# Kernel optimization log

Hardware: AMD Instinct MI355X
Metric: run time of the kernel (lower is better)

Reference implementation:

```python
import jax, jax.numpy as jnp
import numpy as np

# Problem sizes
N, E, G = 100000, 400000, 2048      # nodes, edges, graphs
NIN, H, NHID, NOUT = 300, 256, 512, 768
NL, T = 3, 16                        # extra atom GAT layers (num_layers=4), pooling timesteps
SLOPE = 0.01                         # leaky_relu negative slope (PyG AttentiveFP uses 0.01)


def setup_inputs() -> dict:
    ks = iter(jax.random.split(jax.random.key(0), 80))
    def rn(shape, s=0.1):
        return jax.random.normal(next(ks), shape, dtype=jnp.float32) * s
    inp = {
        "x": rn((N, NIN), 1.0),
        "edge_attr": rn((E, 1), 1.0),
        # learned parameters (inference mode: dropout disabled)
        "lin1_W": rn((H, NIN)), "lin1_b": rn((H,)),
        # GATEConv
        "g_lin1_W": rn((H, H + 1)), "g_lin2_W": rn((H, H)),
        "g_att_l": rn((H,)), "g_att_r": rn((H,)), "g_bias": rn((H,)),
        "gru0_wih": rn((3 * H, H)), "gru0_whh": rn((3 * H, H)),
        "gru0_bih": rn((3 * H,)), "gru0_bhh": rn((3 * H,)),
        # 3 atom GATConv layers (stacked)
        "atom_W": rn((NL, H, H)), "atom_att_src": rn((NL, H)),
        "atom_att_dst": rn((NL, H)), "atom_bias": rn((NL, H)),
        "agru_wih": rn((NL, 3 * H, H)), "agru_whh": rn((NL, 3 * H, H)),
        "agru_bih": rn((NL, 3 * H)), "agru_bhh": rn((NL, 3 * H)),
        # molecule-level GATConv + GRU (16 timesteps)
        "mol_W": rn((H, H)), "mol_att_src": rn((H,)),
        "mol_att_dst": rn((H,)), "mol_bias": rn((H,)),
        "mgru_wih": rn((3 * H, H)), "mgru_whh": rn((3 * H, H)),
        "mgru_bih": rn((3 * H,)), "mgru_bhh": rn((3 * H,)),
        "lin2_W": rn((NHID, H)), "lin2_b": rn((NHID,)),
        "fc1_W": rn((NOUT, NHID)), "fc1_b": rn((NOUT,)),
        # int inputs
        "edge_index": jax.random.randint(next(ks), (2, E), 0, N),
        "batch": jnp.sort(jax.random.randint(next(ks), (N,), 0, G)),
    }
    return inp


def _lrelu(x):
    return jnp.where(x >= 0, x, SLOPE * x)


def _gru(xin, h, wih, whh, bih, bhh):
    gi = xin @ wih.T + bih
    gh = h @ whh.T + bhh
    ir, iz, inn = jnp.split(gi, 3, axis=-1)
    hr, hz, hn = jnp.split(gh, 3, axis=-1)
    r = jax.nn.sigmoid(ir + hr)
    z = jax.nn.sigmoid(iz + hz)
    n = jnp.tanh(inn + r * hn)
    return (1.0 - z) * n + z * h


def _seg_softmax(a, idx, n):
    m = jax.ops.segment_max(a, idx, num_segments=n)
    e = jnp.exp(a - m[idx])
    s = jax.ops.segment_sum(e, idx, num_segments=n)
    return e / s[idx]


def reference(x, edge_attr, lin1_W, lin1_b, g_lin1_W, g_lin2_W, g_att_l, g_att_r,
              g_bias, gru0_wih, gru0_whh, gru0_bih, gru0_bhh, atom_W, atom_att_src,
              atom_att_dst, atom_bias, agru_wih, agru_whh, agru_bih, agru_bhh,
              mol_W, mol_att_src, mol_att_dst, mol_bias, mgru_wih, mgru_whh,
              mgru_bih, mgru_bhh, lin2_W, lin2_b, fc1_W, fc1_b, edge_index, batch):
    src, dst = edge_index[0], edge_index[1]
    # input projection
    x = _lrelu(x @ lin1_W.T + lin1_b)                                   # [N, H]
    # GATEConv: edge-feature attention
    ge = _lrelu(jnp.concatenate([x[src], edge_attr], axis=-1) @ g_lin1_W.T)  # [E, H]
    a = _lrelu(ge @ g_att_l + (x @ g_att_r)[dst])                       # [E]
    alpha = _seg_softmax(a, dst, N)
    h = jax.ops.segment_sum((x[src] @ g_lin2_W.T) * alpha[:, None], dst,
                            num_segments=N) + g_bias
    x = jax.nn.relu(_gru(jax.nn.elu(h), x, gru0_wih, gru0_whh, gru0_bih, gru0_bhh))
    # remaining atom GATConv + GRU layers
    for l in range(NL):
        xw = x @ atom_W[l].T                                            # [N, H]
        a = _lrelu((xw @ atom_att_src[l])[src] + (xw @ atom_att_dst[l])[dst])
        alpha = _seg_softmax(a, dst, N)
        h = jax.ops.segment_sum(xw[src] * alpha[:, None], dst,
                                num_segments=N) + atom_bias[l]
        x = jax.nn.relu(_gru(jax.nn.elu(h), x, agru_wih[l], agru_whh[l],
                             agru_bih[l], agru_bhh[l]))
    # attentive global pooling (node -> graph bipartite GAT, 16 timesteps)
    out = jax.nn.relu(jax.ops.segment_sum(x, batch, num_segments=G))    # [G, H]
    xw = x @ mol_W.T                                                    # shared lin for src/dst
    a_src = xw @ mol_att_src                                            # [N]
    for _ in range(T):
        a = _lrelu(a_src + ((out @ mol_W.T) @ mol_att_dst)[batch])      # [N]
        alpha = _seg_softmax(a, batch, G)
        h = jax.ops.segment_sum(xw * alpha[:, None], batch,
                                num_segments=G) + mol_bias
        out = jax.nn.relu(_gru(jax.nn.elu(h), out, mgru_wih, mgru_whh,
                               mgru_bih, mgru_bhh))
    out = out @ lin2_W.T + lin2_b                                       # [G, NHID]
    # encoder head: relu -> (global_mean_pool is identity on graph-level emb) -> fc1
    return jax.nn.relu(out) @ fc1_W.T + fc1_b                           # [G, NOUT]
```

## Files before the change

kernel.cpp:

```cpp
#include <hip/hip_runtime.h>
#include <hip/hip_bf16.h>
#include <math.h>

typedef __attribute__((ext_vector_type(8))) short           short8;
typedef __attribute__((ext_vector_type(8))) unsigned short  ushort8;
typedef __attribute__((ext_vector_type(4))) unsigned short  us4;
typedef __attribute__((ext_vector_type(4))) float           f32x4;

__device__ __forceinline__ float lreluf(float v){ return v >= 0.f ? v : 0.01f*v; }
__device__ __forceinline__ float sigf(float v){ return 1.f/(1.f + expf(-v)); }

#define OP_NONE  0
#define OP_LRELU 1
#define OP_RELU  2

__device__ __forceinline__ float applyOp(float v, int op){
  if (op == OP_LRELU) return v >= 0.f ? v : 0.01f*v;
  if (op == OP_RELU)  return v > 0.f ? v : 0.f;
  return v;
}

__device__ __forceinline__ unsigned short f2b(float f){
  unsigned x = __float_as_uint(f);
  unsigned lsb = (x >> 16) & 1u;
  return (unsigned short)((x + 0x7fffu + lsb) >> 16);
}
__device__ __forceinline__ float b2f(unsigned short h){
  return __uint_as_float((unsigned)h << 16);
}
__device__ __forceinline__ void split2(float v, unsigned short& h, unsigned short& l){
  h = f2b(v);
  l = f2b(v - b2f(h));
}
__device__ __forceinline__ float rec2(unsigned short h, unsigned short l){
  return b2f(h) + b2f(l);
}

__device__ __forceinline__ int ldsOff(int row, int chunk){
  return row*32 + ((chunk ^ ((row >> 1) & 3)) << 3);
}

__device__ __forceinline__ float blkSum(float v, float* red){
  int t = threadIdx.x;
  red[t] = v; __syncthreads();
  for (int s = 128; s > 0; s >>= 1){ if (t < s) red[t] += red[t+s]; __syncthreads(); }
  float r = red[0]; __syncthreads();
  return r;
}
__device__ __forceinline__ float blkMax(float v, float* red){
  int t = threadIdx.x;
  red[t] = v; __syncthreads();
  for (int s = 128; s > 0; s >>= 1){ if (t < s) red[t] = fmaxf(red[t], red[t+s]); __syncthreads(); }
  float r = red[0]; __syncthreads();
  return r;
}

__device__ __forceinline__ f32x4 mfma3(short8 aH, short8 aL, short8 bH, short8 bL, f32x4 acc){
  acc = __builtin_amdgcn_mfma_f32_16x16x32_bf16(aL, bH, acc, 0, 0, 0);
  acc = __builtin_amdgcn_mfma_f32_16x16x32_bf16(aH, bL, acc, 0, 0, 0);
  acc = __builtin_amdgcn_mfma_f32_16x16x32_bf16(aH, bH, acc, 0, 0, 0);
  return acc;
}

__global__ void wsplit_k(const float* __restrict__ src, unsigned short* __restrict__ Hd,
                         unsigned short* __restrict__ Ld, int lda, int K, long long tot)
{
  long long i = (long long)blockIdx.x*256 + threadIdx.x;
  if (i >= tot) return;
  long long r = i / K; int c = (int)(i % K);
  float v = src[r*lda + c];
  unsigned short h = f2b(v);
  Hd[r*(long long)K + c] = h;
  Ld[r*(long long)K + c] = f2b(v - b2f(h));
}

__device__ __forceinline__ void stagePS(const unsigned short* __restrict__ GH,
    const unsigned short* __restrict__ GL, int ldk, int row0, int k0,
    unsigned short* __restrict__ ldsH, unsigned short* __restrict__ ldsL, int tid)
{
  int r = tid >> 2, c = tid & 3;
  size_t go = (size_t)(row0 + r)*ldk + k0 + c*8;
  ushort8 vh = *(const ushort8*)&GH[go];
  ushort8 vl = *(const ushort8*)&GL[go];
  int off = ldsOff(r, c);
  *(ushort8*)&ldsH[off] = vh;
  *(ushort8*)&ldsL[off] = vl;
}

__device__ __forceinline__ void stage2(const float* __restrict__ src, int lda,
    int row0, int rowmax, int k0, int K,
    unsigned short* __restrict__ ldsH, unsigned short* __restrict__ ldsL, int tid)
{
  int r = tid >> 2, c = tid & 3;
  int gr = row0 + r, gk = k0 + c*8;
  const float* p = src + (size_t)gr*lda + gk;
  float f[8];
  if (gr < rowmax && gk + 8 <= K && ((lda & 3) == 0)){
    float4 f0 = *(const float4*)p;
    float4 f1 = *(const float4*)(p+4);
    f[0]=f0.x; f[1]=f0.y; f[2]=f0.z; f[3]=f0.w;
    f[4]=f1.x; f[5]=f1.y; f[6]=f1.z; f[7]=f1.w;
  } else {
    #pragma unroll
    for (int j = 0; j < 8; ++j) f[j] = (gr < rowmax && gk + j < K) ? p[j] : 0.f;
  }
  ushort8 vh, vl;
  #pragma unroll
  for (int j = 0; j < 8; ++j){
    unsigned short h, l; split2(f[j], h, l);
    vh[j] = h; vl[j] = l;
  }
  int off = ldsOff(r, c);
  *(ushort8*)&ldsH[off] = vh;
  *(ushort8*)&ldsL[off] = vl;
}

__global__ __launch_bounds__(256) void gemm_mfma_k(
    const float* __restrict__ A, int lda,
    const float* __restrict__ W, int ldw,
    const float* __restrict__ bias,
    unsigned short* __restrict__ CH, unsigned short* __restrict__ CL,
    int M, int N, int K, int op)
{
  __shared__ unsigned short AsH[64*32], AsL[64*32];
  __shared__ unsigned short WsH[64*32], WsL[64*32];
  const int tid = threadIdx.x;
  const int bm = blockIdx.y * 64, bn = blockIdx.x * 64;
  const int wave = tid >> 6, lane = tid & 63;
  const int wr = wave >> 1, wc = wave & 1;
  const int quad = lane >> 4, id = lane & 15;

  f32x4 acc[2][2] = {};
  const int iters = (K + 31) / 32;
  for (int kt = 0; kt < iters; ++kt){
    int k0 = kt * 32;
    stage2(A, lda, bm, M, k0, K, AsH, AsL, tid);
    stage2(W, ldw, bn, N, k0, K, WsH, WsL, tid);
    __syncthreads();
    short8 aH[2], aL[2], bH[2], bL[2];
    #pragma unroll
    for (int i = 0; i < 2; ++i){
      int off = ldsOff(wr*32 + i*16 + id, quad);
      aH[i] = *(const short8*)&AsH[off];
      aL[i] = *(const short8*)&AsL[off];
    }
    #pragma unroll
    for (int j = 0; j < 2; ++j){
      int off = ldsOff(wc*32 + j*16 + id, quad);
      bH[j] = *(const short8*)&WsH[off];
      bL[j] = *(const short8*)&WsL[off];
    }
    #pragma unroll
    for (int i = 0; i < 2; ++i)
      #pragma unroll
      for (int j = 0; j < 2; ++j)
        acc[i][j] = mfma3(aH[i], aL[i], bH[j], bL[j], acc[i][j]);
    __syncthreads();
  }
  #pragma unroll
  for (int i = 0; i < 2; ++i){
    int gr0 = bm + wr*32 + i*16 + quad*4;
    #pragma unroll
    for (int j = 0; j < 2; ++j){
      int gc = bn + wc*32 + j*16 + id;
      if (gc >= N) continue;
      float bv = bias ? bias[gc] : 0.f;
      #pragma unroll
      for (int r = 0; r < 4; ++r){
        int row = gr0 + r;
        if (row >= M) continue;
        float v = applyOp(acc[i][j][r] + bv, op);
        unsigned short h, l; split2(v, h, l);
        CH[(size_t)row*N + gc] = h;
        CL[(size_t)row*N + gc] = l;
      }
    }
  }
}

__global__ __launch_bounds__(256) void gemm_ps_k(
    const unsigned short* __restrict__ AH, const unsigned short* __restrict__ AL,
    const unsigned short* __restrict__ WH_, const unsigned short* __restrict__ WL_,
    const float* __restrict__ bias, float* __restrict__ C,
    unsigned short* __restrict__ CH, unsigned short* __restrict__ CL,
    int M, int N, int K, int op, int ncb)
{
  __shared__ unsigned short AsH[64*32], AsL[64*32];
  __shared__ unsigned short WsH[64*32], WsL[64*32];
  int nwg = gridDim.x, bid = blockIdx.x;
  int q = nwg >> 3, r = nwg & 7;
  int xcd = bid & 7, jj = bid >> 3;
  int idx = (xcd < r ? xcd*(q+1) : r*(q+1) + (xcd - r)*q) + jj;
  const int bm = (idx / ncb)*64, bn = (idx % ncb)*64;
  const int tid = threadIdx.x;
  const int wave = tid >> 6, lane = tid & 63;
  const int wr = wave >> 1, wc = wave & 1;
  const int quad = lane >> 4, id = lane & 15;

  f32x4 acc[2][2] = {};
  const int iters = K >> 5;
  for (int kt = 0; kt < iters; ++kt){
    int k0 = kt * 32;
    stagePS(AH, AL, K, bm, k0, AsH, AsL, tid);
    stagePS(WH_, WL_, K, bn, k0, WsH, WsL, tid);
    __syncthreads();
    short8 aH[2], aL[2], bH[2], bL[2];
    #pragma unroll
    for (int i = 0; i < 2; ++i){
      int off = ldsOff(wr*32 + i*16 + id, quad);
      aH[i] = *(const short8*)&AsH[off];
      aL[i] = *(const short8*)&AsL[off];
    }
    #pragma unroll
    for (int j = 0; j < 2; ++j){
      int off = ldsOff(wc*32 + j*16 + id, quad);
      bH[j] = *(const short8*)&WsH[off];
      bL[j] = *(const short8*)&WsL[off];
    }
    #pragma unroll
    for (int i = 0; i < 2; ++i)
      #pragma unroll
      for (int j = 0; j < 2; ++j)
        acc[i][j] = mfma3(aH[i], aL[i], bH[j], bL[j], acc[i][j]);
    __syncthreads();
  }
  #pragma unroll
  for (int i = 0; i < 2; ++i){
    int gr0 = bm + wr*32 + i*16 + quad*4;
    #pragma unroll
    for (int j = 0; j < 2; ++j){
      int gc = bn + wc*32 + j*16 + id;
      float bv = bias ? bias[gc] : 0.f;
      #pragma unroll
      for (int rr = 0; rr < 4; ++rr){
        int row = gr0 + rr;
        if (row >= M) continue;
        float v = applyOp(acc[i][j][rr] + bv, op);
        if (C)  C[(size_t)row*N + gc] = v;
        if (CH){
          unsigned short h, l; split2(v, h, l);
          CH[(size_t)row*N + gc] = h;
          CL[(size_t)row*N + gc] = l;
        }
      }
    }
  }
}

__global__ __launch_bounds__(256) void gemm2_ps_k(
    const unsigned short* __restrict__ AH, const unsigned short* __restrict__ AL,
    const unsigned short* __restrict__ W1H, const unsigned short* __restrict__ W1L,
    const unsigned short* __restrict__ W2H, const unsigned short* __restrict__ W2L,
    unsigned short* __restrict__ YH, unsigned short* __restrict__ YL,
    unsigned short* __restrict__ ZH, unsigned short* __restrict__ ZL, int M)
{
  __shared__ unsigned short AsH[64*32], AsL[64*32];
  __shared__ unsigned short U1H[64*32], U1L[64*32];
  __shared__ unsigned short U2H[64*32], U2L[64*32];
  int nwg = gridDim.x, bid = blockIdx.x;
  int q = nwg >> 3, r = nwg & 7;
  int xcd = bid & 7, jj = bid >> 3;
  int idx = (xcd < r ? xcd*(q+1) : r*(q+1) + (xcd - r)*q) + jj;
  const int bm = (idx >> 2)*64, bn = (idx & 3)*64;
  const int tid = threadIdx.x;
  const int wave = tid >> 6, lane = tid & 63;
  const int wr = wave >> 1, wc = wave & 1;
  const int quad = lane >> 4, id = lane & 15;

  f32x4 acc1[2][2] = {}, acc2[2][2] = {};
  for (int kt = 0; kt < 8; ++kt){
    int k0 = kt * 32;
    stagePS(AH, AL, 256, bm, k0, AsH, AsL, tid);
    stagePS(W1H, W1L, 256, bn, k0, U1H, U1L, tid);
    stagePS(W2H, W2L, 256, bn, k0, U2H, U2L, tid);
    __syncthreads();
    short8 aH[2], aL[2];
    #pragma unroll
    for (int i = 0; i < 2; ++i){
      int off = ldsOff(wr*32 + i*16 + id, quad);
      aH[i] = *(const short8*)&AsH[off];
      aL[i] = *(const short8*)&AsL[off];
    }
    #pragma unroll
    for (int j = 0; j < 2; ++j){
      int off = ldsOff(wc*32 + j*16 + id, quad);
      short8 bh, bl;
      bh = *(const short8*)&U1H[off]; bl = *(const short8*)&U1L[off];
      #pragma unroll
      for (int i = 0; i < 2; ++i) acc1[i][j] = mfma3(aH[i], aL[i], bh, bl, acc1[i][j]);
      bh = *(const short8*)&U2H[off]; bl = *(const short8*)&U2L[off];
      #pragma unroll
      for (int i = 0; i < 2; ++i) acc2[i][j] = mfma3(aH[i], aL[i], bh, bl, acc2[i][j]);
    }
    __syncthreads();
  }
  #pragma unroll
  for (int i = 0; i < 2; ++i){
    int gr0 = bm + wr*32 + i*16 + quad*4;
    #pragma unroll
    for (int j = 0; j < 2; ++j){
      int gc = bn + wc*32 + j*16 + id;
      #pragma unroll
      for (int rr = 0; rr < 4; ++rr){
        int row = gr0 + rr;
        if (row >= M) continue;
        unsigned short h, l;
        split2(acc1[i][j][rr], h, l);
        YH[(size_t)row*256 + gc] = h; YL[(size_t)row*256 + gc] = l;
        split2(acc2[i][j][rr], h, l);
        ZH[(size_t)row*256 + gc] = h; ZL[(size_t)row*256 + gc] = l;
      }
    }
  }
}

__device__ __forceinline__ void gru_phase_ps(
    const unsigned short* __restrict__ AH, const unsigned short* __restrict__ AL,
    const unsigned short* __restrict__ WH_, const unsigned short* __restrict__ WL_,
    int bm, int bn, int tid, int wr, int wc, int quad, int id,
    unsigned short* AsH, unsigned short* AsL,
    unsigned short* W0H, unsigned short* W0L,
    unsigned short* W1H, unsigned short* W1L,
    unsigned short* W2H, unsigned short* W2L,
    f32x4 (&accR)[2][2], f32x4 (&accZ)[2][2], f32x4 (&accN)[2][2])
{
  for (int kt = 0; kt < 8; ++kt){
    int k0 = kt * 32;
    stagePS(AH, AL, 256, bm, k0, AsH, AsL, tid);
    stagePS(WH_,          WL_,          256, bn, k0, W0H, W0L, tid);
    stagePS(WH_ + 65536,  WL_ + 65536,  256, bn, k0, W1H, W1L, tid);
    stagePS(WH_ + 131072, WL_ + 131072, 256, bn, k0, W2H, W2L, tid);
    __syncthreads();
    short8 aH[2], aL[2];
    #pragma unroll
    for (int i = 0; i < 2; ++i){
      int off = ldsOff(wr*32 + i*16 + id, quad);
      aH[i] = *(const short8*)&AsH[off];
      aL[i] = *(const short8*)&AsL[off];
    }
    #pragma unroll
    for (int j = 0; j < 2; ++j){
      int off = ldsOff(wc*32 + j*16 + id, quad);
      short8 bh, bl;
      bh = *(const short8*)&W0H[off]; bl = *(const short8*)&W0L[off];
      #pragma unroll
      for (int i = 0; i < 2; ++i) accR[i][j] = mfma3(aH[i], aL[i], bh, bl, accR[i][j]);
      bh = *(const short8*)&W1H[off]; bl = *(const short8*)&W1L[off];
      #pragma unroll
      for (int i = 0; i < 2; ++i) accZ[i][j] = mfma3(aH[i], aL[i], bh, bl, accZ[i][j]);
      bh = *(const short8*)&W2H[off]; bl = *(const short8*)&W2L[off];
      #pragma unroll
      for (int i = 0; i < 2; ++i) accN[i][j] = mfma3(aH[i], aL[i], bh, bl, accN[i][j]);
    }
    __syncthreads();
  }
}

__global__ __launch_bounds__(256) void gru_ps_k(
    const unsigned short* __restrict__ XinH, const unsigned short* __restrict__ XinL,
    const unsigned short* __restrict__ HidH, const unsigned short* __restrict__ HidL,
    const unsigned short* __restrict__ wihH, const unsigned short* __restrict__ wihL,
    const unsigned short* __restrict__ whhH, const unsigned short* __restrict__ whhL,
    const float* __restrict__ bih, const float* __restrict__ bhh,
    unsigned short* __restrict__ OutH, unsigned short* __restrict__ OutL, int M)
{
  __shared__ unsigned short AsH[64*32], AsL[64*32];
  __shared__ unsigned short W0H[64*32], W0L[64*32];
  __shared__ unsigned short W1H[64*32], W1L[64*32];
  __shared__ unsigned short W2H[64*32], W2L[64*32];
  int nwg = gridDim.x, bid = blockIdx.x;
  int q = nwg >> 3, r = nwg & 7;
  int xcd = bid & 7, jj = bid >> 3;
  int idx = (xcd < r ? xcd*(q+1) : r*(q+1) + (xcd - r)*q) + jj;
  const int bm = (idx >> 2)*64, bn = (idx & 3)*64;
  const int tid = threadIdx.x;
  const int wave = tid >> 6, lane = tid & 63;
  const int wr = wave >> 1, wc = wave & 1;
  const int quad = lane >> 4, id = lane & 15;

  f32x4 accR[2][2] = {}, accZ[2][2] = {}, accI[2][2] = {}, accH[2][2] = {};

  gru_phase_ps(XinH, XinL, wihH, wihL, bm, bn, tid, wr, wc, quad, id,
               AsH, AsL, W0H, W0L, W1H, W1L, W2H, W2L, accR, accZ, accI);
  gru_phase_ps(HidH, HidL, whhH, whhL, bm, bn, tid, wr, wc, quad, id,
               AsH, AsL, W0H, W0L, W1H, W1L, W2H, W2L, accR, accZ, accH);

  #pragma unroll
  for (int i = 0; i < 2; ++i){
    int gr0 = bm + wr*32 + i*16 + quad*4;
    #pragma unroll
    for (int j = 0; j < 2; ++j){
      int gc = bn + wc*32 + j*16 + id;
      float br_  = bih[gc]     + bhh[gc];
      float bz_  = bih[256+gc] + bhh[256+gc];
      float bn_i = bih[512+gc], bn_h = bhh[512+gc];
      #pragma unroll
      for (int rr = 0; rr < 4; ++rr){
        int row = gr0 + rr;
        if (row >= M) continue;
        float rg = sigf(accR[i][j][rr] + br_);
        float zg = sigf(accZ[i][j][rr] + bz_);
        float ng = tanhf(accI[i][j][rr] + bn_i + rg*(accH[i][j][rr] + bn_h));
        float hv = rec2(HidH[(size_t)row*256 + gc], HidL[(size_t)row*256 + gc]);
        float o = (1.f - zg)*ng + zg*hv;
        o = o > 0.f ? o : 0.f;
        unsigned short h, l; split2(o, h, l);
        OutH[(size_t)row*256 + gc] = h;
        OutL[(size_t)row*256 + gc] = l;
      }
    }
  }
}

__global__ __launch_bounds__(256) void rowdot2_ps_k(
    const unsigned short* __restrict__ XH, const unsigned short* __restrict__ XL,
    const float* __restrict__ w1, const float* __restrict__ w2,
    float* __restrict__ y1, float* __restrict__ y2, int M)
{
  int m = blockIdx.x*4 + (threadIdx.x >> 6);
  if (m >= M) return;
  int lane = threadIdx.x & 63;
  us4 vh = *(const us4*)&XH[(size_t)m*256 + lane*4];
  us4 vl = *(const us4*)&XL[(size_t)m*256 + lane*4];
  float p1 = 0.f, p2 = 0.f;
  #pragma unroll
  for (int u = 0; u < 4; ++u){
    float xv = rec2(vh[u], vl[u]);
    int c = lane*4 + u;
    p1 += xv * w1[c];
    if (w2) p2 += xv * w2[c];
  }
  for (int o = 32; o > 0; o >>= 1){
    p1 += __shfl_down(p1, o);
    if (w2) p2 += __shfl_down(p2, o);
  }
  if (lane == 0){ y1[m] = p1; if (w2) y2[m] = p2; }
}

__global__ void hist_k(const int* __restrict__ dst, unsigned* __restrict__ deg, int E){
  int e = blockIdx.x*256 + threadIdx.x;
  if (e >= E) return;
  atomicAdd(&deg[dst[e]], 1u);
}

__global__ __launch_bounds__(256) void scan1_k(const unsigned* __restrict__ deg,
    unsigned* __restrict__ incl, unsigned* __restrict__ bsum, int N)
{
  __shared__ unsigned sm[256];
  int t = threadIdx.x;
  int i = blockIdx.x*256 + t;
  unsigned v = (i < N) ? deg[i] : 0u;
  sm[t] = v; __syncthreads();
  for (int s = 1; s < 256; s <<= 1){
    unsigned u = (t >= s) ? sm[t - s] : 0u;
    __syncthreads();
    sm[t] += u;
    __syncthreads();
  }
  if (i < N) incl[i] = sm[t];
  if (t == 255) bsum[blockIdx.x] = sm[255];
}

__global__ __launch_bounds__(256) void scan2_k(unsigned* __restrict__ bsum, int nb){
  __shared__ unsigned sm[256];
  __shared__ unsigned carry;
  int t = threadIdx.x;
  if (t == 0) carry = 0u;
  __syncthreads();
  for (int base = 0; base < nb; base += 256){
    int i = base + t;
    unsigned v = (i < nb) ? bsum[i] : 0u;
    sm[t] = v; __syncthreads();
    for (int s = 1; s < 256; s <<= 1){
      unsigned u = (t >= s) ? sm[t - s] : 0u;
      __syncthreads();
      sm[t] += u;
      __syncthreads();
    }
    unsigned total = sm[255];
    unsigned c = carry;
    if (i < nb) bsum[i] = c + sm[t] - v;
    __syncthreads();
    if (t == 0) carry = c + total;
    __syncthreads();
  }
}

__global__ void scan3_k(const unsigned* __restrict__ incl, const unsigned* __restrict__ deg,
    const unsigned* __restrict__ bsum, unsigned* __restrict__ off, int N, int E)
{
  int i = blockIdx.x*256 + threadIdx.x;
  if (i < N) off[i] = incl[i] - deg[i] + bsum[blockIdx.x];
  if (i == 0) off[N] = (unsigned)E;
}

__global__ void fill_k(const int* __restrict__ src, const int* __restrict__ dst,
    const unsigned* __restrict__ off, unsigned* __restrict__ cur,
    int* __restrict__ csr_src, int* __restrict__ csr_eid, int E)
{
  int e = blockIdx.x*256 + threadIdx.x;
  if (e >= E) return;
  int d = dst[e];
  unsigned p = off[d] + atomicAdd(&cur[d], 1u);
  csr_src[p] = src[e];
  csr_eid[p] = e;
}

__global__ __launch_bounds__(256) void gate_edge_score_csr_k(
    const unsigned short* __restrict__ YH, const unsigned short* __restrict__ YL,
    const float* __restrict__ g_lin1W,
    const float* __restrict__ att_l, const float* __restrict__ ea_in,
    const float* __restrict__ xr, const int* __restrict__ csr_src,
    const int* __restrict__ csr_eid, const int* __restrict__ dst,
    float* __restrict__ a_out, int E, int H)
{
  int p = blockIdx.x*4 + (threadIdx.x >> 6);
  if (p >= E) return;
  int lane = threadIdx.x & 63;
  int s = csr_src[p];
  int e = csr_eid[p];
  int d = dst[e];
  float eav = ea_in[e];
  us4 vh = *(const us4*)&YH[(size_t)s*256 + lane*4];
  us4 vl = *(const us4*)&YL[(size_t)s*256 + lane*4];
  float acc = 0.f;
  #pragma unroll
  for (int u = 0; u < 4; ++u){
    int c = lane*4 + u;
    float yv = rec2(vh[u], vl[u]) + eav * g_lin1W[(size_t)c*(H+1) + H];
    acc += lreluf(yv) * att_l[c];
  }
  for (int o = 32; o > 0; o >>= 1) acc += __shfl_down(acc, o);
  if (lane == 0) a_out[p] = lreluf(acc + xr[d]);
}

__global__ void node_softmax_k(const unsigned* __restrict__ off, const int* __restrict__ csr_src,
    const float* __restrict__ nd1, const float* __restrict__ nd2,
    float* __restrict__ w, int N, int mode)
{
  int n = blockIdx.x*256 + threadIdx.x;
  if (n >= N) return;
  unsigned p0 = off[n], p1 = off[n+1];
  float m = -INFINITY;
  if (mode){
    float d = nd2[n];
    for (unsigned p = p0; p < p1; ++p){
      float a = lreluf(nd1[csr_src[p]] + d);
      w[p] = a;
      m = fmaxf(m, a);
    }
  } else {
    for (unsigned p = p0; p < p1; ++p) m = fmaxf(m, w[p]);
  }
  float ssum = 0.f;
  for (unsigned p = p0; p < p1; ++p){
    float e = expf(w[p] - m);
    w[p] = e; ssum += e;
  }
  float inv = (ssum > 0.f) ? 1.f/ssum : 0.f;
  for (unsigned p = p0; p < p1; ++p) w[p] *= inv;
}

__global__ __launch_bounds__(256) void gather_h_k(
    const unsigned short* __restrict__ ZH, const unsigned short* __restrict__ ZL,
    const float* __restrict__ w, const unsigned* __restrict__ off,
    const int* __restrict__ csr_src, const float* __restrict__ bias,
    unsigned short* __restrict__ hH, unsigned short* __restrict__ hL, int N)
{
  int n = blockIdx.x*4 + (threadIdx.x >> 6);
  if (n >= N) return;
  int lane = threadIdx.x & 63;
  unsigned p0 = off[n], p1 = off[n+1];
  float4 acc = make_float4(0.f, 0.f, 0.f, 0.f);
  for (unsigned p = p0; p < p1; ++p){
    float wv = w[p];
    size_t zo = (size_t)csr_src[p]*256 + lane*4;
    us4 zh = *(const us4*)&ZH[zo];
    us4 zl = *(const us4*)&ZL[zo];
    acc.x = fmaf(wv, rec2(zh[0], zl[0]), acc.x);
    acc.y = fmaf(wv, rec2(zh[1], zl[1]), acc.y);
    acc.z = fmaf(wv, rec2(zh[2], zl[2]), acc.z);
    acc.w = fmaf(wv, rec2(zh[3], zl[3]), acc.w);
  }
  const float4 b = *(const float4*)&bias[lane*4];
  float vals[4];
  float v;
  v = acc.x + b.x; vals[0] = v > 0.f ? v : expf(v) - 1.f;
  v = acc.y + b.y; vals[1] = v > 0.f ? v : expf(v) - 1.f;
  v = acc.z + b.z; vals[2] = v > 0.f ? v : expf(v) - 1.f;
  v = acc.w + b.w; vals[3] = v > 0.f ? v : expf(v) - 1.f;
  us4 vh, vl;
  #pragma unroll
  for (int u = 0; u < 4; ++u){
    unsigned short h, l; split2(vals[u], h, l);
    vh[u] = h; vl[u] = l;
  }
  *(us4*)&hH[(size_t)n*256 + lane*4] = vh;
  *(us4*)&hL[(size_t)n*256 + lane*4] = vl;
}

__global__ void seg_bounds_k(const int* __restrict__ batch, unsigned* __restrict__ gs,
                             unsigned* __restrict__ ge, int N){
  int n = blockIdx.x*256 + threadIdx.x;
  if (n >= N) return;
  int g = batch[n];
  atomicMin(&gs[g], (unsigned)n);
  atomicMax(&ge[g], (unsigned)(n+1));
}
__global__ __launch_bounds__(256) void graph_pool_k(
    const unsigned short* __restrict__ xH, const unsigned short* __restrict__ xL,
    const unsigned* __restrict__ gs, const unsigned* __restrict__ ge,
    unsigned short* __restrict__ outgH, unsigned short* __restrict__ outgL)
{
  int g = blockIdx.x, t = threadIdx.x;
  unsigned s0 = gs[g], e0 = ge[g];
  float acc = 0.f;
  for (unsigned n = s0; n < e0; ++n)
    acc += rec2(xH[(size_t)n*256 + t], xL[(size_t)n*256 + t]);
  acc = acc > 0.f ? acc : 0.f;
  unsigned short h, l; split2(acc, h, l);
  outgH[(size_t)g*256 + t] = h;
  outgL[(size_t)g*256 + t] = l;
}
__global__ void precompute_v_k(const float* __restrict__ W, const float* __restrict__ ad,
                               float* __restrict__ v){
  int i = threadIdx.x;
  float acc = 0.f;
  for (int j = 0; j < 256; ++j) acc += W[(size_t)j*256 + i] * ad[j];
  v[i] = acc;
}
__global__ __launch_bounds__(256) void mol_pool_k(
    const unsigned short* __restrict__ ogH, const unsigned short* __restrict__ ogL,
    const float* __restrict__ v, const float* __restrict__ asrc,
    const unsigned short* __restrict__ xwH, const unsigned short* __restrict__ xwL,
    const unsigned* __restrict__ gs, const unsigned* __restrict__ geb,
    const float* __restrict__ bias,
    unsigned short* __restrict__ hgH, unsigned short* __restrict__ hgL)
{
  __shared__ float red[256];
  int g = blockIdx.x, t = threadIdx.x;
  float ogv = rec2(ogH[(size_t)g*256 + t], ogL[(size_t)g*256 + t]);
  float tg = blkSum(ogv * v[t], red);
  unsigned s0 = gs[g], e0 = geb[g];
  float mx = -INFINITY;
  for (unsigned n = s0 + t; n < e0; n += 256) mx = fmaxf(mx, lreluf(asrc[n] + tg));
  mx = blkMax(mx, red);
  float sm = 0.f;
  for (unsigned n = s0 + t; n < e0; n += 256) sm += expf(lreluf(asrc[n] + tg) - mx);
  sm = blkSum(sm, red);
  float acc = 0.f;
  if (e0 > s0 && sm > 0.f){
    float inv = 1.f / sm;
    for (unsigned n = s0; n < e0; ++n){
      float w = expf(lreluf(asrc[n] + tg) - mx) * inv;
      acc = fmaf(w, rec2(xwH[(size_t)n*256 + t], xwL[(size_t)n*256 + t]), acc);
    }
  }
  float h0 = acc + bias[t];
  h0 = h0 > 0.f ? h0 : expf(h0) - 1.f;
  unsigned short h, l; split2(h0, h, l);
  hgH[(size_t)g*256 + t] = h;
  hgL[(size_t)g*256 + t] = l;
}

extern "C" void kernel_launch(void* const* d_in, const int* in_sizes, int n_in,
                              void* d_out, int out_size, void* d_ws, size_t ws_size,
                              hipStream_t stream)
{
  (void)n_in; (void)ws_size;
  const int H    = in_sizes[3];
  const int NIN  = in_sizes[2] / H;
  const int N    = in_sizes[0] / NIN;
  const int E    = in_sizes[1];
  const int NL   = in_sizes[16] / H;
  const int NHID = in_sizes[30];
  const int NOUT = in_sizes[32];
  const int G    = out_size / NOUT;
  const int T    = 16;

  const float* x_in     = (const float*)d_in[0];
  const float* ea_in    = (const float*)d_in[1];
  const float* lin1_W   = (const float*)d_in[2];
  const float* lin1_b   = (const float*)d_in[3];
  const float* g_lin1W  = (const float*)d_in[4];
  const float* g_lin2W  = (const float*)d_in[5];
  const float* g_att_l  = (const float*)d_in[6];
  const float* g_att_r  = (const float*)d_in[7];
  const float* g_bias   = (const float*)d_in[8];
  const float* gru0_wih = (const float*)d_in[9];
  const float* gru0_whh = (const float*)d_in[10];
  const float* gru0_bih = (const float*)d_in[11];
  const float* gru0_bhh = (const float*)d_in[12];
  const float* atom_W   = (const float*)d_in[13];
  const float* atom_as  = (const float*)d_in[14];
  const float* atom_ad  = (const float*)d_in[15];
  const float* atom_b   = (const float*)d_in[16];
  const float* agru_wih = (const float*)d_in[17];
  const float* agru_whh = (const float*)d_in[18];
  const float* agru_bih = (const float*)d_in[19];
  const float* agru_bhh = (const float*)d_in[20];
  const float* mol_W    = (const float*)d_in[21];
  const float* mol_as   = (const float*)d_in[22];
  const float* mol_ad   = (const float*)d_in[23];
  const float* mol_b    = (const float*)d_in[24];
  const float* mgru_wih = (const float*)d_in[25];
  const float* mgru_whh = (const float*)d_in[26];
  const float* mgru_bih = (const float*)d_in[27];
  const float* mgru_bhh = (const float*)d_in[28];
  const float* lin2_W   = (const float*)d_in[29];
  const float* lin2_b   = (const float*)d_in[30];
  const float* fc1_W    = (const float*)d_in[31];
  const float* fc1_b    = (const float*)d_in[32];
  const int*  eidx      = (const int*)d_in[33];
  const int*  batch     = (const int*)d_in[34];
  const int*  srcI = eidx;
  const int*  dstI = eidx + E;

  char* wp = (char*)d_ws;
  auto alloc = [&](size_t bytes)->void*{
    void* p = (void*)wp;
    wp += (bytes + 255) & ~(size_t)255;
    return p;
  };
  auto allocUS = [&](size_t elems)->unsigned short*{ return (unsigned short*)alloc(elems*2); };

  unsigned short *xH  = allocUS((size_t)N*H), *xL  = allocUS((size_t)N*H);
  unsigned short *tAH = allocUS((size_t)N*H), *tAL = allocUS((size_t)N*H);
  unsigned short *hbH = allocUS((size_t)N*H), *hbL = allocUS((size_t)N*H);
  float*    ea    = (float*)alloc((size_t)E*4);
  float*    nd1   = (float*)alloc((size_t)N*4);
  float*    nd2   = (float*)alloc((size_t)N*4);
  unsigned short *ogH  = allocUS((size_t)G*H), *ogL  = allocUS((size_t)G*H);
  unsigned short *og2H = allocUS((size_t)G*H), *og2L = allocUS((size_t)G*H);
  unsigned short *hgH  = allocUS((size_t)G*H), *hgL  = allocUS((size_t)G*H);
  unsigned short *o2H  = allocUS((size_t)G*NHID), *o2L = allocUS((size_t)G*NHID);
  unsigned* gsb   = (unsigned*)alloc((size_t)G*4);
  unsigned* geb   = (unsigned*)alloc((size_t)G*4);
  float*    vvec  = (float*)alloc((size_t)H*4);
  const int nb = (N + 255) / 256;
  unsigned* deg     = (unsigned*)alloc((size_t)N*4);
  unsigned* cur     = (unsigned*)alloc((size_t)N*4);
  unsigned* incl    = (unsigned*)alloc((size_t)N*4);
  unsigned* off     = (unsigned*)alloc((size_t)(N+1)*4);
  unsigned* bsum    = (unsigned*)alloc((size_t)nb*4);
  int*      csr_src = (int*)alloc((size_t)E*4);
  int*      csr_eid = (int*)alloc((size_t)E*4);
  const size_t WG = (size_t)768*256;
  const size_t WS = (size_t)256*256;
  unsigned short *g0ihH = allocUS(WG), *g0ihL = allocUS(WG);
  unsigned short *g0hhH = allocUS(WG), *g0hhL = allocUS(WG);
  unsigned short *aihH  = allocUS(WG*NL), *aihL = allocUS(WG*NL);
  unsigned short *ahhH  = allocUS(WG*NL), *ahhL = allocUS(WG*NL);
  unsigned short *mihH  = allocUS(WG), *mihL = allocUS(WG);
  unsigned short *mhhH  = allocUS(WG), *mhhL = allocUS(WG);
  unsigned short *gl1H  = allocUS(WS), *gl1L = allocUS(WS);
  unsigned short *gl2H  = allocUS(WS), *gl2L = allocUS(WS);
  unsigned short *atWH  = allocUS(WS*NL), *atWL = allocUS(WS*NL);
  unsigned short *molH  = allocUS(WS), *molL = allocUS(WS);
  unsigned short *l2WH  = allocUS((size_t)NHID*256), *l2WL = allocUS((size_t)NHID*256);
  unsigned short *f1WH  = allocUS((size_t)NOUT*NHID), *f1WL = allocUS((size_t)NOUT*NHID);

  auto gemmps = [&](const unsigned short* AH_, const unsigned short* AL_,
                    const unsigned short* WH_, const unsigned short* WL_,
                    const float* bias, float* C, unsigned short* CH, unsigned short* CL,
                    int M_, int N_, int K_, int op){
    int ncb = N_ / 64;
    int nwg = ((M_ + 63)/64) * ncb;
    gemm_ps_k<<<dim3(nwg), dim3(256), 0, stream>>>(AH_, AL_, WH_, WL_, bias, C, CH, CL,
                                                   M_, N_, K_, op, ncb);
  };
  auto grup = [&](const unsigned short* XiH, const unsigned short* XiL,
                  const unsigned short* HiH, const unsigned short* HiL,
                  const unsigned short* ihH, const unsigned short* ihL,
                  const unsigned short* hhH, const unsigned short* hhL,
                  const float* bih, const float* bhh,
                  unsigned short* OH, unsigned short* OL, int M_){
    int nwg = ((M_ + 63)/64)*4;
    gru_ps_k<<<dim3(nwg), dim3(256), 0, stream>>>(XiH, XiL, HiH, HiL,
                                                  ihH, ihL, hhH, hhL, bih, bhh,
                                                  OH, OL, M_);
  };
  auto wsplit = [&](const float* src, unsigned short* Hd, unsigned short* Ld,
                    int lda, int K, long long rows){
    long long tot = rows * K;
    wsplit_k<<<dim3((unsigned)((tot + 255)/256)), dim3(256), 0, stream>>>(src, Hd, Ld, lda, K, tot);
  };

  wsplit(gru0_wih, g0ihH, g0ihL, 256, 256, 768);
  wsplit(gru0_whh, g0hhH, g0hhL, 256, 256, 768);
  wsplit(agru_wih, aihH, aihL, 256, 256, (long long)NL*768);
  wsplit(agru_whh, ahhH, ahhL, 256, 256, (long long)NL*768);
  wsplit(mgru_wih, mihH, mihL, 256, 256, 768);
  wsplit(mgru_whh, mhhH, mhhL, 256, 256, 768);
  wsplit(g_lin1W,  gl1H, gl1L, H+1, 256, 256);
  wsplit(g_lin2W,  gl2H, gl2L, 256, 256, 256);
  wsplit(atom_W,   atWH, atWL, 256, 256, (long long)NL*256);
  wsplit(mol_W,    molH, molL, 256, 256, 256);
  wsplit(lin2_W,   l2WH, l2WL, 256, 256, NHID);
  wsplit(fc1_W,    f1WH, f1WL, NHID, NHID, NOUT);

  hipMemsetAsync(deg, 0, (size_t)N*4, stream);
  hist_k<<<dim3((E+255)/256), dim3(256), 0, stream>>>(dstI, deg, E);
  scan1_k<<<dim3(nb), dim3(256), 0, stream>>>(deg, incl, bsum, N);
  scan2_k<<<dim3(1), dim3(256), 0, stream>>>(bsum, nb);
  scan3_k<<<dim3(nb), dim3(256), 0, stream>>>(incl, deg, bsum, off, N, E);
  hipMemsetAsync(cur, 0, (size_t)N*4, stream);
  fill_k<<<dim3((E+255)/256), dim3(256), 0, stream>>>(srcI, dstI, off, cur, csr_src, csr_eid, E);

  {
    dim3 gr(4, (N + 63)/64);
    gemm_mfma_k<<<gr, dim3(256), 0, stream>>>(x_in, NIN, lin1_W, NIN, lin1_b,
                                              xH, xL, N, H, NIN, OP_LRELU);
  }

  {
    int nwg = ((N + 63)/64)*4;
    gemm2_ps_k<<<dim3(nwg), dim3(256), 0, stream>>>(xH, xL, gl1H, gl1L, gl2H, gl2L,
                                                    hbH, hbL, tAH, tAL, N);
  }
  rowdot2_ps_k<<<dim3((N+3)/4), dim3(256), 0, stream>>>(xH, xL, g_att_r, (const float*)nullptr,
                                                        nd1, (float*)nullptr, N);
  gate_edge_score_csr_k<<<dim3((E+3)/4), dim3(256), 0, stream>>>(hbH, hbL, g_lin1W, g_att_l,
                                                                 ea_in, nd1, csr_src, csr_eid,
                                                                 dstI, ea, E, H);
  node_softmax_k<<<dim3(nb), dim3(256), 0, stream>>>(off, csr_src, nullptr, nullptr, ea, N, 0);
  gather_h_k<<<dim3((N+3)/4), dim3(256), 0, stream>>>(tAH, tAL, ea, off, csr_src, g_bias,
                                                      hbH, hbL, N);
  grup(hbH, hbL, xH, xL, g0ihH, g0ihL, g0hhH, g0hhL, gru0_bih, gru0_bhh, tAH, tAL, N);
  { unsigned short* t = xH; xH = tAH; tAH = t; t = xL; xL = tAL; tAL = t; }

  for (int l = 0; l < NL; ++l){
    gemmps(xH, xL, atWH + (size_t)l*WS, atWL + (size_t)l*WS, nullptr,
           nullptr, tAH, tAL, N, 256, 256, OP_NONE);
    rowdot2_ps_k<<<dim3((N+3)/4), dim3(256), 0, stream>>>(tAH, tAL, atom_as + (size_t)l*H,
                                                          atom_ad + (size_t)l*H, nd1, nd2, N);
    node_softmax_k<<<dim3(nb), dim3(256), 0, stream>>>(off, csr_src, nd1, nd2, ea, N, 1);
    gather_h_k<<<dim3((N+3)/4), dim3(256), 0, stream>>>(tAH, tAL, ea, off, csr_src,
                                                        atom_b + (size_t)l*H, hbH, hbL, N);
    grup(hbH, hbL, xH, xL,
         aihH + (size_t)l*WG, aihL + (size_t)l*WG,
         ahhH + (size_t)l*WG, ahhL + (size_t)l*WG,
         agru_bih + (size_t)l*3*H, agru_bhh + (size_t)l*3*H, tAH, tAL, N);
    { unsigned short* t = xH; xH = tAH; tAH = t; t = xL; xL = tAL; tAL = t; }
  }

  hipMemsetAsync(gsb, 0xFF, (size_t)G*4, stream);
  hipMemsetAsync(geb, 0x00, (size_t)G*4, stream);
  seg_bounds_k<<<dim3((N+255)/256), dim3(256), 0, stream>>>(batch, gsb, geb, N);
  graph_pool_k<<<dim3(G), dim3(256), 0, stream>>>(xH, xL, gsb, geb, ogH, ogL);
  gemmps(xH, xL, molH, molL, nullptr, nullptr, tAH, tAL, N, 256, 256, OP_NONE);
  rowdot2_ps_k<<<dim3((N+3)/4), dim3(256), 0, stream>>>(tAH, tAL, mol_as, (const float*)nullptr,
                                                        nd1, (float*)nullptr, N);
  precompute_v_k<<<dim3(1), dim3(256), 0, stream>>>(mol_W, mol_ad, vvec);
  unsigned short *cogH = ogH, *cogL = ogL, *cog2H = og2H, *cog2L = og2L;
  for (int t = 0; t < T; ++t){
    mol_pool_k<<<dim3(G), dim3(256), 0, stream>>>(cogH, cogL, vvec, nd1, tAH, tAL,
                                                  gsb, geb, mol_b, hgH, hgL);
    grup(hgH, hgL, cogH, cogL, mihH, mihL, mhhH, mhhL, mgru_bih, mgru_bhh,
         cog2H, cog2L, G);
    { unsigned short* tt = cogH; cogH = cog2H; cog2H = tt;
      tt = cogL; cogL = cog2L; cog2L = tt; }
  }

  gemmps(cogH, cogL, l2WH, l2WL, lin2_b, nullptr, o2H, o2L, G, NHID, 256, OP_RELU);
  gemmps(o2H, o2L, f1WH, f1WL, fc1_b, (float*)d_out, nullptr, nullptr, G, NOUT, NHID, OP_NONE);
}
```

Baseline: 3.996 ms.

## Use direct global-to-LDS loads, source-grouped edge scoring, and prefetch in gather

Several unrelated changes land together. Weight/activation staging in stagePS now uses global_load_lds with an XOR-swizzled column to bypass registers. A second CSC-style index (edges grouped by source) is built so the GATE edge-score kernel loads each source row once and loops over its outgoing edges. gather_h_k software-prefetches the next neighbour row. The extra CSC build adds several small kernels, and the source-major scoring writes scattered outputs with uneven per-wave work.

```diff
diff --git a/kernel.cpp b/kernel.cpp
--- a/kernel.cpp
+++ b/kernel.cpp
@@ -13,6 +13,10 @@
 #define OP_NONE  0
 #define OP_LRELU 1
 #define OP_RELU  2
+
+#define GLDS16(gp, lp) __builtin_amdgcn_global_load_lds( \
+    (const __attribute__((address_space(1))) void*)(gp), \
+    (__attribute__((address_space(3))) void*)(lp), 16, 0, 0)
 
 __device__ __forceinline__ float applyOp(float v, int op){
   if (op == OP_LRELU) return v >= 0.f ? v : 0.01f*v;
@@ -78,13 +82,12 @@
     const unsigned short* __restrict__ GL, int ldk, int row0, int k0,
     unsigned short* __restrict__ ldsH, unsigned short* __restrict__ ldsL, int tid)
 {
-  int r = tid >> 2, c = tid & 3;
+  int r = tid >> 2;
+  int c = (tid & 3) ^ ((r >> 1) & 3);
   size_t go = (size_t)(row0 + r)*ldk + k0 + c*8;
-  ushort8 vh = *(const ushort8*)&GH[go];
-  ushort8 vl = *(const ushort8*)&GL[go];
-  int off = ldsOff(r, c);
-  *(ushort8*)&ldsH[off] = vh;
-  *(ushort8*)&ldsL[off] = vl;
+  int wbase = (tid >> 6) * 512;
+  GLDS16(&GH[go], &ldsH[wbase]);
+  GLDS16(&GL[go], &ldsL[wbase]);
 }
 
 __device__ __forceinline__ void stage2(const float* __restrict__ src, int lda,
@@ -437,10 +440,10 @@
   if (lane == 0){ y1[m] = p1; if (w2) y2[m] = p2; }
 }
 
-__global__ void hist_k(const int* __restrict__ dst, unsigned* __restrict__ deg, int E){
+__global__ void hist_k(const int* __restrict__ key, unsigned* __restrict__ deg, int E){
   int e = blockIdx.x*256 + threadIdx.x;
   if (e >= E) return;
-  atomicAdd(&deg[dst[e]], 1u);
+  atomicAdd(&deg[key[e]], 1u);
 }
 
 __global__ __launch_bounds__(256) void scan1_k(const unsigned* __restrict__ deg,
@@ -496,7 +499,7 @@
 
 __global__ void fill_k(const int* __restrict__ src, const int* __restrict__ dst,
     const unsigned* __restrict__ off, unsigned* __restrict__ cur,
-    int* __restrict__ csr_src, int* __restrict__ csr_eid, int E)
+    int* __restrict__ csr_src, int* __restrict__ csr_eid, int* __restrict__ epos, int E)
 {
   int e = blockIdx.x*256 + threadIdx.x;
   if (e >= E) return;
@@ -504,34 +507,56 @@
   unsigned p = off[d] + atomicAdd(&cur[d], 1u);
   csr_src[p] = src[e];
   csr_eid[p] = e;
-}
-
-__global__ __launch_bounds__(256) void gate_edge_score_csr_k(
+  epos[e] = (int)p;
+}
+
+__global__ void fill2_k(const int* __restrict__ src, const int* __restrict__ epos,
+    const unsigned* __restrict__ off2, unsigned* __restrict__ cur,
+    int* __restrict__ csc_pos, int E)
+{
+  int e = blockIdx.x*256 + threadIdx.x;
+  if (e >= E) return;
+  int s = src[e];
+  unsigned qq = off2[s] + atomicAdd(&cur[s], 1u);
+  csc_pos[qq] = epos[e];
+}
+
+__global__ __launch_bounds__(256) void gate_edge_score_csc_k(
     const unsigned short* __restrict__ YH, const unsigned short* __restrict__ YL,
     const float* __restrict__ g_lin1W,
     const float* __restrict__ att_l, const float* __restrict__ ea_in,
-    const float* __restrict__ xr, const int* __restrict__ csr_src,
+    const float* __restrict__ xr,
+    const unsigned* __restrict__ off2, const int* __restrict__ csc_pos,
     const int* __restrict__ csr_eid, const int* __restrict__ dst,
-    float* __restrict__ a_out, int E, int H)
-{
-  int p = blockIdx.x*4 + (threadIdx.x >> 6);
-  if (p >= E) return;
+    float* __restrict__ a_out, int N, int H)
+{
+  int s = blockIdx.x*4 + (threadIdx.x >> 6);
+  if (s >= N) return;
   int lane = threadIdx.x & 63;
-  int s = csr_src[p];
-  int e = csr_eid[p];
-  int d = dst[e];
-  float eav = ea_in[e];
+  unsigned q0 = off2[s], q1 = off2[s+1];
+  if (q0 == q1) return;
   us4 vh = *(const us4*)&YH[(size_t)s*256 + lane*4];
   us4 vl = *(const us4*)&YL[(size_t)s*256 + lane*4];
-  float acc = 0.f;
+  float y4[4], w4[4], a4[4];
   #pragma unroll
   for (int u = 0; u < 4; ++u){
     int c = lane*4 + u;
-    float yv = rec2(vh[u], vl[u]) + eav * g_lin1W[(size_t)c*(H+1) + H];
-    acc += lreluf(yv) * att_l[c];
-  }
-  for (int o = 32; o > 0; o >>= 1) acc += __shfl_down(acc, o);
-  if (lane == 0) a_out[p] = lreluf(acc + xr[d]);
+    y4[u] = rec2(vh[u], vl[u]);
+    w4[u] = g_lin1W[(size_t)c*(H+1) + H];
+    a4[u] = att_l[c];
+  }
+  for (unsigned qq = q0; qq < q1; ++qq){
+    int p = csc_pos[qq];
+    int e = csr_eid[p];
+    int d = dst[e];
+    float eav = ea_in[e];
+    float acc = 0.f;
+    #pragma unroll
+    for (int u = 0; u < 4; ++u)
+      acc += lreluf(y4[u] + eav * w4[u]) * a4[u];
+    for (int o = 32; o > 0; o >>= 1) acc += __shfl_down(acc, o);
+    if (lane == 0) a_out[p] = lreluf(acc + xr[d]);
+  }
 }
 
 __global__ void node_softmax_k(const unsigned* __restrict__ off, const int* __restrict__ csr_src,
@@ -572,15 +597,25 @@
   int lane = threadIdx.x & 63;
   unsigned p0 = off[n], p1 = off[n+1];
   float4 acc = make_float4(0.f, 0.f, 0.f, 0.f);
-  for (unsigned p = p0; p < p1; ++p){
-    float wv = w[p];
-    size_t zo = (size_t)csr_src[p]*256 + lane*4;
-    us4 zh = *(const us4*)&ZH[zo];
-    us4 zl = *(const us4*)&ZL[zo];
-    acc.x = fmaf(wv, rec2(zh[0], zl[0]), acc.x);
-    acc.y = fmaf(wv, rec2(zh[1], zl[1]), acc.y);
-    acc.z = fmaf(wv, rec2(zh[2], zl[2]), acc.z);
-    acc.w = fmaf(wv, rec2(zh[3], zl[3]), acc.w);
+  if (p0 < p1){
+    size_t zo = (size_t)csr_src[p0]*256 + lane*4;
+    us4 zh_n = *(const us4*)&ZH[zo];
+    us4 zl_n = *(const us4*)&ZL[zo];
+    float w_n = w[p0];
+    for (unsigned p = p0; p < p1; ++p){
+      us4 zh = zh_n, zl = zl_n;
+      float wv = w_n;
+      if (p + 1 < p1){
+        size_t zo2 = (size_t)csr_src[p+1]*256 + lane*4;
+        zh_n = *(const us4*)&ZH[zo2];
+        zl_n = *(const us4*)&ZL[zo2];
+        w_n = w[p+1];
+      }
+      acc.x = fmaf(wv, rec2(zh[0], zl[0]), acc.x);
+      acc.y = fmaf(wv, rec2(zh[1], zl[1]), acc.y);
+      acc.z = fmaf(wv, rec2(zh[2], zl[2]), acc.z);
+      acc.w = fmaf(wv, rec2(zh[3], zl[3]), acc.w);
+    }
   }
   const float4 b = *(const float4*)&bias[lane*4];
   float vals[4];
@@ -742,9 +777,12 @@
   unsigned* cur     = (unsigned*)alloc((size_t)N*4);
   unsigned* incl    = (unsigned*)alloc((size_t)N*4);
   unsigned* off     = (unsigned*)alloc((size_t)(N+1)*4);
+  unsigned* off2    = (unsigned*)alloc((size_t)(N+1)*4);
   unsigned* bsum    = (unsigned*)alloc((size_t)nb*4);
   int*      csr_src = (int*)alloc((size_t)E*4);
   int*      csr_eid = (int*)alloc((size_t)E*4);
+  int*      epos    = (int*)alloc((size_t)E*4);
+  int*      csc_pos = (int*)alloc((size_t)E*4);
   const size_t WG = (size_t)768*256;
   const size_t WS = (size_t)256*256;
   unsigned short *g0ihH = allocUS(WG), *g0ihL = allocUS(WG);
@@ -805,7 +843,14 @@
   scan2_k<<<dim3(1), dim3(256), 0, stream>>>(bsum, nb);
   scan3_k<<<dim3(nb), dim3(256), 0, stream>>>(incl, deg, bsum, off, N, E);
   hipMemsetAsync(cur, 0, (size_t)N*4, stream);
-  fill_k<<<dim3((E+255)/256), dim3(256), 0, stream>>>(srcI, dstI, off, cur, csr_src, csr_eid, E);
+  fill_k<<<dim3((E+255)/256), dim3(256), 0, stream>>>(srcI, dstI, off, cur, csr_src, csr_eid, epos, E);
+  hipMemsetAsync(deg, 0, (size_t)N*4, stream);
+  hist_k<<<dim3((E+255)/256), dim3(256), 0, stream>>>(srcI, deg, E);
+  scan1_k<<<dim3(nb), dim3(256), 0, stream>>>(deg, incl, bsum, N);
+  scan2_k<<<dim3(1), dim3(256), 0, stream>>>(bsum, nb);
+  scan3_k<<<dim3(nb), dim3(256), 0, stream>>>(incl, deg, bsum, off2, N, E);
+  hipMemsetAsync(cur, 0, (size_t)N*4, stream);
+  fill2_k<<<dim3((E+255)/256), dim3(256), 0, stream>>>(srcI, epos, off2, cur, csc_pos, E);
 
   {
     dim3 gr(4, (N + 63)/64);
@@ -820,9 +865,9 @@
   }
   rowdot2_ps_k<<<dim3((N+3)/4), dim3(256), 0, stream>>>(xH, xL, g_att_r, (const float*)nullptr,
                                                         nd1, (float*)nullptr, N);
-  gate_edge_score_csr_k<<<dim3((E+3)/4), dim3(256), 0, stream>>>(hbH, hbL, g_lin1W, g_att_l,
-                                                                 ea_in, nd1, csr_src, csr_eid,
-                                                                 dstI, ea, E, H);
+  gate_edge_score_csc_k<<<dim3((N+3)/4), dim3(256), 0, stream>>>(hbH, hbL, g_lin1W, g_att_l,
+                                                                 ea_in, nd1, off2, csc_pos,
+                                                                 csr_eid, dstI, ea, N, H);
   node_softmax_k<<<dim3(nb), dim3(256), 0, stream>>>(off, csr_src, nullptr, nullptr, ea, N, 0);
   gather_h_k<<<dim3((N+3)/4), dim3(256), 0, stream>>>(tAH, tAL, ea, off, csr_src, g_bias,
                                                       hbH, hbL, N);
```

Measured after the change: 3.893 ms. -2.6%, faster.
